# Optimization experiments

Hardware: AMD Instinct MI355X
Metric: run time of the kernel (lower is better)

## Reference

```python
import jax, jax.numpy as jnp
import numpy as np

N, E = 50000, 800000
NFEAT, HID, NHEAD, NCLASS = 256, 32, 8, 40
NEG_SLOPE = 0.2


def gat_conv(x, src, dst, W, a_src, a_dst, bias, heads, out_ch, concat):
    n = x.shape[0]
    h = (x @ W).reshape(n, heads, out_ch)              # [N, H, C]
    alpha_src = jnp.einsum('nhc,hc->nh', h, a_src)     # [N, H]
    alpha_dst = jnp.einsum('nhc,hc->nh', h, a_dst)
    e = jax.nn.leaky_relu(alpha_src[src] + alpha_dst[dst], NEG_SLOPE)  # [E, H]
    # segment softmax over incoming edges of each dst node
    m = jax.ops.segment_max(e, dst, num_segments=n)
    ex = jnp.exp(e - m[dst])
    s = jax.ops.segment_sum(ex, dst, num_segments=n)
    alpha = ex / (s[dst] + 1e-16)                      # [E, H]
    out = jax.ops.segment_sum(h[src] * alpha[:, :, None], dst, num_segments=n)  # [N, H, C]
    out = out.reshape(n, heads * out_ch) if concat else out.mean(axis=1)
    return out + bias


def setup_inputs() -> dict:
    key = jax.random.key(0)
    ks = jax.random.split(key, 12)
    x = jax.random.normal(ks[0], (N, NFEAT), dtype=jnp.float32)
    edge_index = jax.random.randint(ks[1], (2, E), 0, N, dtype=jnp.int64)
    edge_attr = jax.random.normal(ks[2], (E, 8), dtype=jnp.float32)  # unused by the model
    s1 = 1.0 / np.sqrt(NFEAT)
    s2 = 1.0 / np.sqrt(HID * NHEAD)
    W1 = jax.random.normal(ks[3], (NFEAT, NHEAD * HID), dtype=jnp.float32) * s1
    att_src1 = jax.random.normal(ks[4], (NHEAD, HID), dtype=jnp.float32) * 0.1
    att_dst1 = jax.random.normal(ks[5], (NHEAD, HID), dtype=jnp.float32) * 0.1
    b1 = jnp.zeros((NHEAD * HID,), dtype=jnp.float32)
    W2 = jax.random.normal(ks[6], (NHEAD * HID, NCLASS), dtype=jnp.float32) * s2
    att_src2 = jax.random.normal(ks[7], (1, NCLASS), dtype=jnp.float32) * 0.1
    att_dst2 = jax.random.normal(ks[8], (1, NCLASS), dtype=jnp.float32) * 0.1
    b2 = jnp.zeros((NCLASS,), dtype=jnp.float32)
    return {"x": x, "edge_index": edge_index, "edge_attr": edge_attr,
            "W1": W1, "att_src1": att_src1, "att_dst1": att_dst1, "b1": b1,
            "W2": W2, "att_src2": att_src2, "att_dst2": att_dst2, "b2": b2}


def reference(x, edge_index, edge_attr, W1, att_src1, att_dst1, b1, W2, att_src2, att_dst2, b2):
    # eval mode: dropout is identity. GATConv adds self-loops by default.
    n = x.shape[0]
    loops = jnp.arange(n, dtype=edge_index.dtype)
    src = jnp.concatenate([edge_index[0], loops])
    dst = jnp.concatenate([edge_index[1], loops])
    h = jax.nn.elu(gat_conv(x, src, dst, W1, att_src1, att_dst1, b1, NHEAD, HID, True))
    final = gat_conv(h, src, dst, W2, att_src2, att_dst2, b2, 1, NCLASS, False)
    return final, jax.nn.log_softmax(final, axis=1)
```

## Files before the change

### kernel.cpp

```cpp
#include <hip/hip_runtime.h>
#include <hip/hip_bf16.h>
#include <math.h>

#define NN 50000
#define EE 800000
#define ET 850000
#define F1 256
#define NHEAD 8
#define HID 32
#define NCLASS 40
#define NEG 0.2f

typedef __attribute__((ext_vector_type(8))) short short8_t;
typedef __attribute__((ext_vector_type(4))) float float4_t;

__device__ __forceinline__ int clampN(int v) {
    return v < 0 ? 0 : (v >= NN ? NN - 1 : v);
}
__device__ __forceinline__ unsigned short f2bf(float f) {
    __hip_bfloat16 h = __float2bfloat16(f);
    return __builtin_bit_cast(unsigned short, h);
}
__device__ __forceinline__ float bf2f(unsigned short u) {
    return __uint_as_float((unsigned)u << 16);
}

__global__ __launch_bounds__(256) void hist_kernel(const int* __restrict__ ei, int* __restrict__ deg) {
    int t = blockIdx.x * 256 + threadIdx.x;
    if (t >= ET) return;
    int d = (t < EE) ? ei[EE + t] : (t - EE);
    d = clampN(d);
    atomicAdd(&deg[d], 1);
}

__global__ __launch_bounds__(256) void scan1_kernel(const int* __restrict__ deg, int* __restrict__ off, int* __restrict__ bsum) {
    __shared__ int lds[256];
    int b = blockIdx.x, tid = threadIdx.x;
    int base = b * 1024 + tid * 4;
    int v0 = (base + 0 < NN) ? deg[base + 0] : 0;
    int v1 = (base + 1 < NN) ? deg[base + 1] : 0;
    int v2 = (base + 2 < NN) ? deg[base + 2] : 0;
    int v3 = (base + 3 < NN) ? deg[base + 3] : 0;
    int s1 = v0 + v1, s2 = s1 + v2, s3 = s2 + v3;
    lds[tid] = s3;
    __syncthreads();
    for (int o = 1; o < 256; o <<= 1) {
        int t = (tid >= o) ? lds[tid - o] : 0;
        __syncthreads();
        if (tid >= o) lds[tid] += t;
        __syncthreads();
    }
    int excl = tid ? lds[tid - 1] : 0;
    if (base + 0 < NN) off[base + 1] = excl + v0;
    if (base + 1 < NN) off[base + 2] = excl + s1;
    if (base + 2 < NN) off[base + 3] = excl + s2;
    if (base + 3 < NN) off[base + 4] = excl + s3;
    if (tid == 255) bsum[b] = lds[255];
}

__global__ __launch_bounds__(256) void scan2_kernel(int* __restrict__ bsum, int nb) {
    __shared__ int lds[256];
    int tid = threadIdx.x;
    lds[tid] = (tid < nb) ? bsum[tid] : 0;
    __syncthreads();
    for (int o = 1; o < 256; o <<= 1) {
        int t = (tid >= o) ? lds[tid - o] : 0;
        __syncthreads();
        if (tid >= o) lds[tid] += t;
        __syncthreads();
    }
    if (tid < nb) bsum[tid] = lds[tid];
}

__global__ __launch_bounds__(256) void scan3_kernel(int* __restrict__ off, const int* __restrict__ bsum) {
    int b = blockIdx.x, tid = threadIdx.x;
    if (b == 0 && tid == 0) off[0] = 0;
    if (b == 0) return;
    int add = bsum[b - 1];
    int base = b * 1024 + tid * 4;
    #pragma unroll
    for (int i = 0; i < 4; ++i) {
        if (base + i < NN) off[base + i + 1] += add;
    }
}

__global__ __launch_bounds__(256) void scatter_kernel(const int* __restrict__ ei, const int* __restrict__ off,
                                                      int* __restrict__ cursor, int* __restrict__ esrc) {
    int t = blockIdx.x * 256 + threadIdx.x;
    if (t >= ET) return;
    int s, d;
    if (t < EE) { s = ei[t]; d = ei[EE + t]; }
    else        { s = t - EE; d = t - EE; }
    s = clampN(s); d = clampN(d);
    int p = off[d] + atomicAdd(&cursor[d], 1);
    esrc[p] = s;
}

__global__ __launch_bounds__(256) void prep_kernel(const float* __restrict__ W1,
                                                   const float* __restrict__ as1, const float* __restrict__ ad1,
                                                   unsigned short* __restrict__ Bh, unsigned short* __restrict__ Bl) {
    int n = blockIdx.x;
    int k = threadIdx.x;
    float v;
    if (n < 256) {
        v = W1[(size_t)k * 256 + n];
    } else {
        int j = n - 256;
        int h = j & 7;
        const float* att = (j < 8) ? (as1 + h * 32) : (ad1 + h * 32);
        float s = 0.f;
        #pragma unroll
        for (int c = 0; c < 32; ++c) s += W1[(size_t)k * 256 + h * 32 + c] * att[c];
        v = s;
    }
    unsigned short hi = f2bf(v);
    Bh[n * 256 + k] = hi;
    Bl[n * 256 + k] = f2bf(v - bf2f(hi));
}

#define AKP 40
__global__ __launch_bounds__(256, 2) void gemm1_kernel(const float* __restrict__ x,
                                                       const unsigned short* __restrict__ Bh,
                                                       const unsigned short* __restrict__ Bl,
                                                       unsigned short* __restrict__ h1b,
                                                       float* __restrict__ asrc1, float* __restrict__ adst1) {
    __shared__ __align__(16) unsigned short Ah[128 * AKP];
    __shared__ __align__(16) unsigned short Al[128 * AKP];
    __shared__ __align__(16) unsigned short Bhs[272 * AKP];
    __shared__ __align__(16) unsigned short Bls[272 * AKP];
    int tid = threadIdx.x;
    int wave = tid >> 6, lane = tid & 63;
    int quad = lane >> 4, l16 = lane & 15;
    int row0 = blockIdx.x * 128;

    float4_t acc[2][17];
    #pragma unroll
    for (int i = 0; i < 2; ++i)
        #pragma unroll
        for (int j = 0; j < 17; ++j) acc[i][j] = (float4_t){0.f, 0.f, 0.f, 0.f};

    for (int k0 = 0; k0 < 256; k0 += 32) {
        __syncthreads();
        #pragma unroll
        for (int i = 0; i < 4; ++i) {
            int id = i * 256 + tid;
            int r = id >> 3, kq = id & 7;
            int rr = row0 + r; if (rr >= NN) rr = NN - 1;
            float4 v = *(const float4*)(x + (size_t)rr * 256 + k0 + kq * 4);
            ushort4 hi, lo;
            hi.x = f2bf(v.x); lo.x = f2bf(v.x - bf2f(hi.x));
            hi.y = f2bf(v.y); lo.y = f2bf(v.y - bf2f(hi.y));
            hi.z = f2bf(v.z); lo.z = f2bf(v.z - bf2f(hi.z));
            hi.w = f2bf(v.w); lo.w = f2bf(v.w - bf2f(hi.w));
            *(ushort4*)(Ah + r * AKP + kq * 4) = hi;
            *(ushort4*)(Al + r * AKP + kq * 4) = lo;
        }
        for (int id = tid; id < 272 * 4; id += 256) {
            int r = id >> 2, kq = id & 3;
            *(float4*)(Bhs + r * AKP + kq * 8) = *(const float4*)(Bh + (size_t)r * 256 + k0 + kq * 8);
            *(float4*)(Bls + r * AKP + kq * 8) = *(const float4*)(Bl + (size_t)r * 256 + k0 + kq * 8);
        }
        __syncthreads();
        short8_t ah[2], al[2];
        #pragma unroll
        for (int mt = 0; mt < 2; ++mt) {
            int mrow = wave * 32 + mt * 16 + l16;
            ah[mt] = *(const short8_t*)(Ah + mrow * AKP + quad * 8);
            al[mt] = *(const short8_t*)(Al + mrow * AKP + quad * 8);
        }
        #pragma unroll
        for (int nt = 0; nt < 17; ++nt) {
            int nrow = nt * 16 + l16;
            short8_t bh  = *(const short8_t*)(Bhs + nrow * AKP + quad * 8);
            short8_t blo = *(const short8_t*)(Bls + nrow * AKP + quad * 8);
            #pragma unroll
            for (int mt = 0; mt < 2; ++mt) {
                acc[mt][nt] = __builtin_amdgcn_mfma_f32_16x16x32_bf16(ah[mt], bh,  acc[mt][nt], 0, 0, 0);
                acc[mt][nt] = __builtin_amdgcn_mfma_f32_16x16x32_bf16(ah[mt], blo, acc[mt][nt], 0, 0, 0);
                acc[mt][nt] = __builtin_amdgcn_mfma_f32_16x16x32_bf16(al[mt], bh,  acc[mt][nt], 0, 0, 0);
            }
        }
    }
    #pragma unroll
    for (int mt = 0; mt < 2; ++mt) {
        int rbase = row0 + wave * 32 + mt * 16 + quad * 4;
        #pragma unroll
        for (int r = 0; r < 4; ++r) {
            int row = rbase + r;
            if (row >= NN) continue;
            #pragma unroll
            for (int nt = 0; nt < 16; ++nt)
                h1b[(size_t)row * 256 + nt * 16 + l16] = f2bf(acc[mt][nt][r]);
            float v = acc[mt][16][r];
            if (l16 < 8) asrc1[row * 8 + l16] = v;
            else         adst1[row * 8 + (l16 - 8)] = v;
        }
    }
}

__global__ __launch_bounds__(256) void agg1_kernel(const unsigned short* __restrict__ h1b, const float* __restrict__ asrc,
                                                   const float* __restrict__ adst, const int* __restrict__ esrc,
                                                   const int* __restrict__ off,
                                                   const float* __restrict__ b1, float* __restrict__ hout) {
    __shared__ __align__(8) float2 pairs[4][64];
    int tid = threadIdx.x;
    int wave = tid >> 6;
    int wid = blockIdx.x * 4 + wave;
    if (wid >= NN) return;
    int lane = tid & 63;
    int hp = lane & 7;
    int jp = lane >> 3;
    int hc = lane >> 3;
    int c0 = lane * 4;
    float adh_p = adst[wid * 8 + hp];
    int e0 = off[wid], e1 = off[wid + 1];
    const char* hb = (const char*)h1b + ((size_t)c0 << 1);

    float m = -INFINITY, s = 0.f;
    float ax = 0.f, ay = 0.f, az = 0.f, aw = 0.f;

    for (int base = e0; base < e1; base += 64) {
        int cnt = e1 - base; if (cnt > 64) cnt = 64;
        int snv = esrc[base + (lane < cnt ? lane : cnt - 1)];
        int nch = (cnt + 7) >> 3;
        for (int cj = 0; cj < nch; ++cj) {
            int jedge = cj * 8 + jp;
            int sj = __shfl(snv, jedge);
            float a = asrc[sj * 8 + hp];
            float e = a + adh_p;
            e = (e >= 0.f) ? e : NEG * e;
            if (jedge >= cnt) e = -INFINITY;
            float cm = e;
            cm = fmaxf(cm, __shfl_xor(cm, 8));
            cm = fmaxf(cm, __shfl_xor(cm, 16));
            cm = fmaxf(cm, __shfl_xor(cm, 32));
            float mn = fmaxf(m, cm);
            float t = __expf(m - mn);
            float w = __expf(e - mn);
            s = s * t + w;
            m = mn;
            pairs[wave][lane] = make_float2(w, __int_as_float(sj));
            float rrc = __shfl(t, hc);
            ax *= rrc; ay *= rrc; az *= rrc; aw *= rrc;
            const float2* rp = &pairs[wave][hc];
            #pragma unroll
            for (int j = 0; j < 8; ++j) {
                float2 pr = rp[j * 8];
                float wj = pr.x;
                int sj2 = __float_as_int(pr.y);
                uint2 u = *(const uint2*)(hb + ((size_t)(unsigned)sj2 << 9));
                ax += wj * __uint_as_float(u.x << 16);
                ay += wj * __uint_as_float(u.x & 0xFFFF0000u);
                az += wj * __uint_as_float(u.y << 16);
                aw += wj * __uint_as_float(u.y & 0xFFFF0000u);
            }
        }
    }
    s += __shfl_xor(s, 8);
    s += __shfl_xor(s, 16);
    s += __shfl_xor(s, 32);
    float sh = __shfl(s, hc);
    float inv = 1.f / (sh + 1e-16f);
    float4 b = *(const float4*)(b1 + c0);
    float vx = ax * inv + b.x, vy = ay * inv + b.y, vz = az * inv + b.z, vw = aw * inv + b.w;
    float4 o;
    o.x = (vx > 0.f) ? vx : expm1f(vx);
    o.y = (vy > 0.f) ? vy : expm1f(vy);
    o.z = (vz > 0.f) ? vz : expm1f(vz);
    o.w = (vw > 0.f) ? vw : expm1f(vw);
    *(float4*)(hout + (size_t)wid * 256 + c0) = o;
}

#define G2_TM 128
#define G2_KC 32
__global__ __launch_bounds__(256) void gemm2_kernel(const float* __restrict__ h, const float* __restrict__ W2,
                                                    const float* __restrict__ at_s, const float* __restrict__ at_d,
                                                    unsigned short* __restrict__ h2b, float* __restrict__ as2,
                                                    float* __restrict__ ad2) {
    __shared__ __align__(16) float w2s[256 * 40];
    __shared__ __align__(16) float As[G2_KC][132];
    int tid = threadIdx.x;
    for (int i = tid; i < 256 * 40; i += 256) w2s[i] = W2[i];
    int g  = tid & 7;
    int rg = tid >> 3;
    int row0 = blockIdx.x * G2_TM;
    float acc[4][5] = {};
    float ats[5], atd[5];
    #pragma unroll
    for (int j = 0; j < 5; ++j) { ats[j] = at_s[g + 8 * j]; atd[j] = at_d[g + 8 * j]; }

    for (int k0 = 0; k0 < 256; k0 += G2_KC) {
        __syncthreads();
        #pragma unroll
        for (int i = 0; i < 4; ++i) {
            int id = i * 256 + tid;
            int r  = id >> 3;
            int kq = id & 7;
            int rr = row0 + r; if (rr >= NN) rr = NN - 1;
            float4 v = *(const float4*)(h + (size_t)rr * 256 + k0 + kq * 4);
            As[kq * 4 + 0][r] = v.x;
            As[kq * 4 + 1][r] = v.y;
            As[kq * 4 + 2][r] = v.z;
            As[kq * 4 + 3][r] = v.w;
        }
        __syncthreads();
        #pragma unroll 4
        for (int k = 0; k < G2_KC; ++k) {
            float4 a = *(const float4*)(&As[k][rg * 4]);
            float w[5];
            #pragma unroll
            for (int j = 0; j < 5; ++j) w[j] = w2s[(k0 + k) * 40 + g + 8 * j];
            float av[4] = {a.x, a.y, a.z, a.w};
            #pragma unroll
            for (int r = 0; r < 4; ++r)
                #pragma unroll
                for (int j = 0; j < 5; ++j)
                    acc[r][j] += av[r] * w[j];
        }
    }

    #pragma unroll
    for (int r = 0; r < 4; ++r) {
        int row = row0 + rg * 4 + r;
        float ps = 0.f, pd = 0.f;
        #pragma unroll
        for (int j = 0; j < 5; ++j) {
            ps += acc[r][j] * ats[j];
            pd += acc[r][j] * atd[j];
        }
        ps += __shfl_xor(ps, 1); pd += __shfl_xor(pd, 1);
        ps += __shfl_xor(ps, 2); pd += __shfl_xor(pd, 2);
        ps += __shfl_xor(ps, 4); pd += __shfl_xor(pd, 4);
        if (row < NN) {
            #pragma unroll
            for (int j = 0; j < 5; ++j) h2b[(size_t)row * 40 + g + 8 * j] = f2bf(acc[r][j]);
            if (g == 0) { as2[row] = ps; ad2[row] = pd; }
        }
    }
}

__global__ __launch_bounds__(256) void agg2_kernel(const unsigned short* __restrict__ h2b, const float* __restrict__ asrc,
                                                   const float* __restrict__ adst, const int* __restrict__ esrc,
                                                   const int* __restrict__ off,
                                                   const float* __restrict__ b2, float* __restrict__ outF,
                                                   float* __restrict__ outL) {
    __shared__ __align__(8) float2 pw2[4][64];
    int tid = threadIdx.x;
    int wave = tid >> 6;
    int wid = blockIdx.x * 4 + wave;
    if (wid >= NN) return;
    int lane = tid & 63;
    int c = lane;
    float adh = adst[wid];
    int e0 = off[wid], e1 = off[wid + 1];
    const char* hb = (const char*)h2b + ((unsigned)(c < NCLASS ? c : 0) << 1);

    float m = -INFINITY, s = 0.f, acc = 0.f;

    for (int base = e0; base < e1; base += 64) {
        int cnt = e1 - base; if (cnt > 64) cnt = 64;
        int snv = esrc[base + (lane < cnt ? lane : cnt - 1)];
        float a = asrc[snv];
        float e = a + adh;
        e = (e >= 0.f) ? e : NEG * e;
        if (lane >= cnt) e = -INFINITY;
        float cm = e;
        cm = fmaxf(cm, __shfl_xor(cm, 1));
        cm = fmaxf(cm, __shfl_xor(cm, 2));
        cm = fmaxf(cm, __shfl_xor(cm, 4));
        cm = fmaxf(cm, __shfl_xor(cm, 8));
        cm = fmaxf(cm, __shfl_xor(cm, 16));
        cm = fmaxf(cm, __shfl_xor(cm, 32));
        float mn = fmaxf(m, cm);
        float t = __expf(m - mn);
        float w = __expf(e - mn);
        s = s * t + w;
        m = mn;
        pw2[wave][lane] = make_float2(w, __int_as_float(snv));
        acc *= t;
        #pragma unroll 1
        for (int j0 = 0; j0 < 64; j0 += 16) {
            if (j0 >= cnt) break;
            #pragma unroll
            for (int j = 0; j < 16; ++j) {
                float2 pr = pw2[wave][j0 + j];
                float wj = pr.x;
                int sj = __float_as_int(pr.y);
                unsigned short hv = *(const unsigned short*)(hb + (unsigned)sj * 80);
                acc += wj * bf2f(hv);
            }
        }
    }
    s += __shfl_xor(s, 1);
    s += __shfl_xor(s, 2);
    s += __shfl_xor(s, 4);
    s += __shfl_xor(s, 8);
    s += __shfl_xor(s, 16);
    s += __shfl_xor(s, 32);
    float inv = 1.f / (s + 1e-16f);
    float fin = (c < NCLASS) ? (acc * inv + b2[c]) : -INFINITY;
    if (c < NCLASS) outF[(size_t)wid * 40 + c] = fin;
    float mx = fin;
    for (int o = 32; o; o >>= 1) mx = fmaxf(mx, __shfl_xor(mx, o));
    float ex = (c < NCLASS) ? __expf(fin - mx) : 0.f;
    float sm = ex;
    for (int o = 32; o; o >>= 1) sm += __shfl_xor(sm, o);
    if (c < NCLASS) outL[(size_t)wid * 40 + c] = fin - mx - __logf(sm);
}

extern "C" void kernel_launch(void* const* d_in, const int* in_sizes, int n_in,
                              void* d_out, int out_size, void* d_ws, size_t ws_size,
                              hipStream_t stream) {
    const float* x   = (const float*)d_in[0];
    const int*   ei  = (const int*)d_in[1];
    const float* W1  = (const float*)d_in[3];
    const float* as1 = (const float*)d_in[4];
    const float* ad1 = (const float*)d_in[5];
    const float* b1  = (const float*)d_in[6];
    const float* W2  = (const float*)d_in[7];
    const float* as2c = (const float*)d_in[8];
    const float* ad2c = (const float*)d_in[9];
    const float* b2  = (const float*)d_in[10];

    float* outF = (float*)d_out;
    float* outL = outF + (size_t)NN * NCLASS;

    char* w = (char*)d_ws;
    auto alloc = [&](size_t bytes) {
        void* p = (void*)w;
        w += (bytes + 255) & ~(size_t)255;
        return p;
    };
    unsigned short* h1b = (unsigned short*)alloc((size_t)NN * 256 * 2);
    float* hbuf  = (float*)alloc((size_t)NN * 256 * 4);
    unsigned short* h2b = (unsigned short*)alloc((size_t)NN * 40 * 2);
    float* asrc1 = (float*)alloc((size_t)NN * 8 * 4);
    float* adst1 = (float*)alloc((size_t)NN * 8 * 4);
    float* asrc2 = (float*)alloc((size_t)NN * 4);
    float* adst2 = (float*)alloc((size_t)NN * 4);
    int* deg    = (int*)alloc((size_t)NN * 4);
    int* off    = (int*)alloc((size_t)(NN + 1) * 4);
    int* cursor = (int*)alloc((size_t)NN * 4);
    int* esrc   = (int*)alloc((size_t)ET * 4);
    int* bsum   = (int*)alloc(64 * 4);
    unsigned short* W1th = (unsigned short*)alloc((size_t)272 * 256 * 2);
    unsigned short* W1tl = (unsigned short*)alloc((size_t)272 * 256 * 2);

    const int NB_SCAN = (NN + 1023) / 1024;

    hipMemsetAsync(deg, 0, (size_t)NN * 4, stream);
    hipMemsetAsync(cursor, 0, (size_t)NN * 4, stream);

    hist_kernel<<<(ET + 255) / 256, 256, 0, stream>>>(ei, deg);
    scan1_kernel<<<NB_SCAN, 256, 0, stream>>>(deg, off, bsum);
    scan2_kernel<<<1, 256, 0, stream>>>(bsum, NB_SCAN);
    scan3_kernel<<<NB_SCAN, 256, 0, stream>>>(off, bsum);
    scatter_kernel<<<(ET + 255) / 256, 256, 0, stream>>>(ei, off, cursor, esrc);

    prep_kernel<<<272, 256, 0, stream>>>(W1, as1, ad1, W1th, W1tl);
    gemm1_kernel<<<(NN + 127) / 128, 256, 0, stream>>>(x, W1th, W1tl, h1b, asrc1, adst1);
    agg1_kernel<<<(NN + 3) / 4, 256, 0, stream>>>(h1b, asrc1, adst1, esrc, off, b1, hbuf);
    gemm2_kernel<<<(NN + G2_TM - 1) / G2_TM, 256, 0, stream>>>(hbuf, W2, as2c, ad2c, h2b, asrc2, adst2);
    agg2_kernel<<<(NN + 3) / 4, 256, 0, stream>>>(h2b, asrc2, adst2, esrc, off, b2, outF, outL);
}
```

Baseline: 376.4 us.

## Restructure GAT aggregation to per-chunk softmax and store hidden layer in bf16

The layer-1 aggregation now computes the max over a whole 64-edge chunk once, instead of rescaling after every 8-edge group. Weights are staged per head in padded shared memory and gathered four edges at a time with vector LDS loads. The intermediate hidden activation is written as bf16 instead of fp32, and gemm2 unpacks it, which halves that buffer's write and read traffic. Layer-2 aggregation gets the same four-wide split weight and index loads. The cost is extra bf16 rounding of the hidden layer and more registers for the per-chunk edge values.

Result: no change. 373.9 us (-0.7%).

```diff
diff --git a/kernel.cpp b/kernel.cpp
--- a/kernel.cpp
+++ b/kernel.cpp
@@ -198,11 +198,13 @@
     }
 }
 
+#define WST 68
 __global__ __launch_bounds__(256) void agg1_kernel(const unsigned short* __restrict__ h1b, const float* __restrict__ asrc,
                                                    const float* __restrict__ adst, const int* __restrict__ esrc,
                                                    const int* __restrict__ off,
-                                                   const float* __restrict__ b1, float* __restrict__ hout) {
-    __shared__ __align__(8) float2 pairs[4][64];
+                                                   const float* __restrict__ b1, unsigned short* __restrict__ hout) {
+    __shared__ __align__(16) float wl[4][8 * WST];
+    __shared__ __align__(16) int  snl[4][64];
     int tid = threadIdx.x;
     int wave = tid >> 6;
     int wid = blockIdx.x * 4 + wave;
@@ -214,7 +216,10 @@
     int c0 = lane * 4;
     float adh_p = adst[wid * 8 + hp];
     int e0 = off[wid], e1 = off[wid + 1];
-    const char* hb = (const char*)h1b + ((size_t)c0 << 1);
+    float* wlw = wl[wave];
+    int* snw = snl[wave];
+    const char* hb = (const char*)h1b;
+    unsigned lofs = (unsigned)c0 * 2;
 
     float m = -INFINITY, s = 0.f;
     float ax = 0.f, ay = 0.f, az = 0.f, aw = 0.f;
@@ -222,38 +227,62 @@
     for (int base = e0; base < e1; base += 64) {
         int cnt = e1 - base; if (cnt > 64) cnt = 64;
         int snv = esrc[base + (lane < cnt ? lane : cnt - 1)];
+        snw[lane] = snv;
         int nch = (cnt + 7) >> 3;
-        for (int cj = 0; cj < nch; ++cj) {
+        float ee[8];
+        float wmax = -INFINITY;
+        #pragma unroll
+        for (int cj = 0; cj < 8; ++cj) {
+            if (cj >= nch) { ee[cj] = -INFINITY; continue; }
             int jedge = cj * 8 + jp;
             int sj = __shfl(snv, jedge);
             float a = asrc[sj * 8 + hp];
             float e = a + adh_p;
             e = (e >= 0.f) ? e : NEG * e;
             if (jedge >= cnt) e = -INFINITY;
-            float cm = e;
-            cm = fmaxf(cm, __shfl_xor(cm, 8));
-            cm = fmaxf(cm, __shfl_xor(cm, 16));
-            cm = fmaxf(cm, __shfl_xor(cm, 32));
-            float mn = fmaxf(m, cm);
-            float t = __expf(m - mn);
-            float w = __expf(e - mn);
-            s = s * t + w;
-            m = mn;
-            pairs[wave][lane] = make_float2(w, __int_as_float(sj));
-            float rrc = __shfl(t, hc);
-            ax *= rrc; ay *= rrc; az *= rrc; aw *= rrc;
-            const float2* rp = &pairs[wave][hc];
-            #pragma unroll
-            for (int j = 0; j < 8; ++j) {
-                float2 pr = rp[j * 8];
-                float wj = pr.x;
-                int sj2 = __float_as_int(pr.y);
-                uint2 u = *(const uint2*)(hb + ((size_t)(unsigned)sj2 << 9));
-                ax += wj * __uint_as_float(u.x << 16);
-                ay += wj * __uint_as_float(u.x & 0xFFFF0000u);
-                az += wj * __uint_as_float(u.y << 16);
-                aw += wj * __uint_as_float(u.y & 0xFFFF0000u);
-            }
+            ee[cj] = e;
+            wmax = fmaxf(wmax, e);
+        }
+        wmax = fmaxf(wmax, __shfl_xor(wmax, 8));
+        wmax = fmaxf(wmax, __shfl_xor(wmax, 16));
+        wmax = fmaxf(wmax, __shfl_xor(wmax, 32));
+        float mn = fmaxf(m, wmax);
+        float t = __expf(m - mn);
+        m = mn;
+        s *= t;
+        float tc = __shfl(t, hc);
+        ax *= tc; ay *= tc; az *= tc; aw *= tc;
+        #pragma unroll
+        for (int cj = 0; cj < 8; ++cj) {
+            if (cj >= nch) break;
+            float w = __expf(ee[cj] - mn);
+            s += w;
+            wlw[hp * WST + cj * 8 + jp] = w;
+        }
+        const float* wrow = wlw + hc * WST;
+        for (int j = 0; j < cnt; j += 4) {
+            float4 w4 = *(const float4*)(wrow + j);
+            int4 sn4 = *(const int4*)(snw + j);
+            uint2 u0 = *(const uint2*)(hb + (((unsigned)sn4.x << 9) + lofs));
+            uint2 u1 = *(const uint2*)(hb + (((unsigned)sn4.y << 9) + lofs));
+            uint2 u2 = *(const uint2*)(hb + (((unsigned)sn4.z << 9) + lofs));
+            uint2 u3 = *(const uint2*)(hb + (((unsigned)sn4.w << 9) + lofs));
+            ax += w4.x * __uint_as_float(u0.x << 16);
+            ay += w4.x * __uint_as_float(u0.x & 0xFFFF0000u);
+            az += w4.x * __uint_as_float(u0.y << 16);
+            aw += w4.x * __uint_as_float(u0.y & 0xFFFF0000u);
+            ax += w4.y * __uint_as_float(u1.x << 16);
+            ay += w4.y * __uint_as_float(u1.x & 0xFFFF0000u);
+            az += w4.y * __uint_as_float(u1.y << 16);
+            aw += w4.y * __uint_as_float(u1.y & 0xFFFF0000u);
+            ax += w4.z * __uint_as_float(u2.x << 16);
+            ay += w4.z * __uint_as_float(u2.x & 0xFFFF0000u);
+            az += w4.z * __uint_as_float(u2.y << 16);
+            aw += w4.z * __uint_as_float(u2.y & 0xFFFF0000u);
+            ax += w4.w * __uint_as_float(u3.x << 16);
+            ay += w4.w * __uint_as_float(u3.x & 0xFFFF0000u);
+            az += w4.w * __uint_as_float(u3.y << 16);
+            aw += w4.w * __uint_as_float(u3.y & 0xFFFF0000u);
         }
     }
     s += __shfl_xor(s, 8);
@@ -263,17 +292,17 @@
     float inv = 1.f / (sh + 1e-16f);
     float4 b = *(const float4*)(b1 + c0);
     float vx = ax * inv + b.x, vy = ay * inv + b.y, vz = az * inv + b.z, vw = aw * inv + b.w;
-    float4 o;
-    o.x = (vx > 0.f) ? vx : expm1f(vx);
-    o.y = (vy > 0.f) ? vy : expm1f(vy);
-    o.z = (vz > 0.f) ? vz : expm1f(vz);
-    o.w = (vw > 0.f) ? vw : expm1f(vw);
-    *(float4*)(hout + (size_t)wid * 256 + c0) = o;
+    ushort4 o;
+    o.x = f2bf((vx > 0.f) ? vx : expm1f(vx));
+    o.y = f2bf((vy > 0.f) ? vy : expm1f(vy));
+    o.z = f2bf((vz > 0.f) ? vz : expm1f(vz));
+    o.w = f2bf((vw > 0.f) ? vw : expm1f(vw));
+    *(ushort4*)(hout + (size_t)wid * 256 + c0) = o;
 }
 
 #define G2_TM 128
 #define G2_KC 32
-__global__ __launch_bounds__(256) void gemm2_kernel(const float* __restrict__ h, const float* __restrict__ W2,
+__global__ __launch_bounds__(256) void gemm2_kernel(const unsigned short* __restrict__ h, const float* __restrict__ W2,
                                                     const float* __restrict__ at_s, const float* __restrict__ at_d,
                                                     unsigned short* __restrict__ h2b, float* __restrict__ as2,
                                                     float* __restrict__ ad2) {
@@ -292,16 +321,20 @@
     for (int k0 = 0; k0 < 256; k0 += G2_KC) {
         __syncthreads();
         #pragma unroll
-        for (int i = 0; i < 4; ++i) {
+        for (int i = 0; i < 2; ++i) {
             int id = i * 256 + tid;
-            int r  = id >> 3;
-            int kq = id & 7;
+            int r  = id >> 2;
+            int kq = id & 3;
             int rr = row0 + r; if (rr >= NN) rr = NN - 1;
-            float4 v = *(const float4*)(h + (size_t)rr * 256 + k0 + kq * 4);
-            As[kq * 4 + 0][r] = v.x;
-            As[kq * 4 + 1][r] = v.y;
-            As[kq * 4 + 2][r] = v.z;
-            As[kq * 4 + 3][r] = v.w;
+            uint4 u = *(const uint4*)(h + (size_t)rr * 256 + k0 + kq * 8);
+            As[kq * 8 + 0][r] = __uint_as_float(u.x << 16);
+            As[kq * 8 + 1][r] = __uint_as_float(u.x & 0xFFFF0000u);
+            As[kq * 8 + 2][r] = __uint_as_float(u.y << 16);
+            As[kq * 8 + 3][r] = __uint_as_float(u.y & 0xFFFF0000u);
+            As[kq * 8 + 4][r] = __uint_as_float(u.z << 16);
+            As[kq * 8 + 5][r] = __uint_as_float(u.z & 0xFFFF0000u);
+            As[kq * 8 + 6][r] = __uint_as_float(u.w << 16);
+            As[kq * 8 + 7][r] = __uint_as_float(u.w & 0xFFFF0000u);
         }
         __syncthreads();
         #pragma unroll 4
@@ -344,7 +377,8 @@
                                                    const int* __restrict__ off,
                                                    const float* __restrict__ b2, float* __restrict__ outF,
                                                    float* __restrict__ outL) {
-    __shared__ __align__(8) float2 pw2[4][64];
+    __shared__ __align__(16) float wl2[4][64];
+    __shared__ __align__(16) int  snl2[4][64];
     int tid = threadIdx.x;
     int wave = tid >> 6;
     int wid = blockIdx.x * 4 + wave;
@@ -354,12 +388,15 @@
     float adh = adst[wid];
     int e0 = off[wid], e1 = off[wid + 1];
     const char* hb = (const char*)h2b + ((unsigned)(c < NCLASS ? c : 0) << 1);
+    float* wlw = wl2[wave];
+    int* snw = snl2[wave];
 
     float m = -INFINITY, s = 0.f, acc = 0.f;
 
     for (int base = e0; base < e1; base += 64) {
         int cnt = e1 - base; if (cnt > 64) cnt = 64;
         int snv = esrc[base + (lane < cnt ? lane : cnt - 1)];
+        snw[lane] = snv;
         float a = asrc[snv];
         float e = a + adh;
         e = (e >= 0.f) ? e : NEG * e;
@@ -376,19 +413,19 @@
         float w = __expf(e - mn);
         s = s * t + w;
         m = mn;
-        pw2[wave][lane] = make_float2(w, __int_as_float(snv));
+        wlw[lane] = w;
         acc *= t;
-        #pragma unroll 1
-        for (int j0 = 0; j0 < 64; j0 += 16) {
-            if (j0 >= cnt) break;
-            #pragma unroll
-            for (int j = 0; j < 16; ++j) {
-                float2 pr = pw2[wave][j0 + j];
-                float wj = pr.x;
-                int sj = __float_as_int(pr.y);
-                unsigned short hv = *(const unsigned short*)(hb + (unsigned)sj * 80);
-                acc += wj * bf2f(hv);
-            }
+        for (int j = 0; j < cnt; j += 4) {
+            float4 w4 = *(const float4*)(wlw + j);
+            int4 sn4 = *(const int4*)(snw + j);
+            unsigned short v0 = *(const unsigned short*)(hb + (unsigned)sn4.x * 80);
+            unsigned short v1 = *(const unsigned short*)(hb + (unsigned)sn4.y * 80);
+            unsigned short v2 = *(const unsigned short*)(hb + (unsigned)sn4.z * 80);
+            unsigned short v3 = *(const unsigned short*)(hb + (unsigned)sn4.w * 80);
+            acc += w4.x * bf2f(v0);
+            acc += w4.y * bf2f(v1);
+            acc += w4.z * bf2f(v2);
+            acc += w4.w * bf2f(v3);
         }
     }
     s += __shfl_xor(s, 1);
@@ -432,7 +469,7 @@
         return p;
     };
     unsigned short* h1b = (unsigned short*)alloc((size_t)NN * 256 * 2);
-    float* hbuf  = (float*)alloc((size_t)NN * 256 * 4);
+    unsigned short* hbuf = (unsigned short*)alloc((size_t)NN * 256 * 2);
     unsigned short* h2b = (unsigned short*)alloc((size_t)NN * 40 * 2);
     float* asrc1 = (float*)alloc((size_t)NN * 8 * 4);
     float* adst1 = (float*)alloc((size_t)NN * 8 * 4);
```
